# Performance work log

Measured on AMD Instinct MI355X. Metric: run time of the kernel, lower is better.

Reference implementation:

```python
import jax, jax.numpy as jnp
import numpy as np
import math

IN_CH = 1024
OUT_CH = 1024
QK_DIM = 512
NHEADS = 8
NDIM = QK_DIM // NHEADS  # 64 per-head qk dim
VDIM = OUT_CH // NHEADS  # 128 per-head value dim
SCALE = 1.0 / math.sqrt(NDIM)


def setup_inputs() -> dict:
    key = jax.random.key(0)
    ks = jax.random.split(key, 7)
    B, N = 4, 2048
    x = jax.random.normal(ks[0], (B, N, IN_CH), dtype=jnp.float32)
    # Linear weights stored as [in, out] so y = x @ W + b
    s_in = 1.0 / math.sqrt(IN_CH)
    Wq = jax.random.uniform(ks[1], (IN_CH, QK_DIM), jnp.float32, -s_in, s_in)
    bq = jax.random.uniform(ks[2], (QK_DIM,), jnp.float32, -s_in, s_in)
    Wk = jax.random.uniform(ks[3], (IN_CH, QK_DIM), jnp.float32, -s_in, s_in)
    bk = jax.random.uniform(ks[4], (QK_DIM,), jnp.float32, -s_in, s_in)
    Wv = jax.random.uniform(ks[5], (IN_CH, OUT_CH), jnp.float32, -s_in, s_in)
    bv = jax.random.uniform(ks[6], (OUT_CH,), jnp.float32, -s_in, s_in)
    return {"x": x, "Wq": Wq, "bq": bq, "Wk": Wk, "bk": bk, "Wv": Wv, "bv": bv}


def reference(x, Wq, bq, Wk, bk, Wv, bv):
    B, N, C = x.shape
    Q = (x @ Wq + bq).reshape(B, N, NHEADS, NDIM)
    K = (x @ Wk + bk).reshape(B, N, NHEADS, NDIM)
    V = (x @ Wv + bv).reshape(B, N, NHEADS, VDIM)
    # scores: [B, H, N, N]
    scores = jnp.einsum("bnhd,bmhd->bhnm", Q, K) * SCALE
    attn = jax.nn.softmax(scores, axis=-1)
    # message: [B, N, H, VDIM] -> [B, N, OUT_CH]
    msg = jnp.einsum("bhnm,bmhv->bnhv", attn, V)
    return msg.reshape(B, N, OUT_CH)
```

## Files before the change

kernel.cpp:

```cpp
#include <hip/hip_runtime.h>
#include <hip/hip_bf16.h>
#include <math.h>


using bf16 = __hip_bfloat16;
typedef __attribute__((ext_vector_type(4))) short bf16x4;
typedef __attribute__((ext_vector_type(8))) short short8;
typedef __attribute__((ext_vector_type(4))) float f32x4;
typedef __attribute__((ext_vector_type(16))) float f32x16;
typedef __attribute__((ext_vector_type(2))) unsigned int uintx2;

#define C2 0.18033688011112042f

__device__ __forceinline__ void async_ld16(const void* g, void* l) {
  __builtin_amdgcn_global_load_lds(
      (const __attribute__((address_space(1))) unsigned int*)g,
      (__attribute__((address_space(3))) unsigned int*)l, 16, 0, 0);
}

__global__ __launch_bounds__(256) void convert_x(const float* __restrict__ x,
                                                 bf16* __restrict__ xb)
{
  const int i = (blockIdx.x * 256 + threadIdx.x) * 8;
  const float4 a = *(const float4*)(x + i);
  const float4 b = *(const float4*)(x + i + 4);
  union { bf16 h[8]; short8 s; } u;
  u.h[0] = __float2bfloat16(a.x); u.h[1] = __float2bfloat16(a.y);
  u.h[2] = __float2bfloat16(a.z); u.h[3] = __float2bfloat16(a.w);
  u.h[4] = __float2bfloat16(b.x); u.h[5] = __float2bfloat16(b.y);
  u.h[6] = __float2bfloat16(b.z); u.h[7] = __float2bfloat16(b.w);
  *(short8*)(xb + i) = u.s;
}

__global__ __launch_bounds__(256) void transpose_weights(
    const float* __restrict__ Wq, const float* __restrict__ Wk,
    const float* __restrict__ Wv, bf16* __restrict__ Wt)
{
  __shared__ __align__(16) bf16 t[32][33];
  const int i0 = blockIdx.x * 32;
  const int o0 = blockIdx.y * 32;
  const int tx = threadIdx.x & 31, ty = threadIdx.x >> 5;
#pragma unroll
  for (int s = 0; s < 32; s += 8) {
    const int i = i0 + ty + s;
    const int o = o0 + tx;
    const float w = (o < 512)  ? Wq[(size_t)i * 512 + o]
                  : (o < 1024) ? Wk[(size_t)i * 512 + (o - 512)]
                               : Wv[(size_t)i * 1024 + (o - 1024)];
    t[ty + s][tx] = __float2bfloat16(w);
  }
  __syncthreads();
#pragma unroll
  for (int s = 0; s < 32; s += 8)
    Wt[(size_t)(o0 + ty + s) * 1024 + i0 + tx] = t[tx][ty + s];
}

__global__ __launch_bounds__(256, 2) void qkv_gemm(
    const bf16* __restrict__ xb, const bf16* __restrict__ Wt,
    const float* __restrict__ bq, const float* __restrict__ bk,
    const float* __restrict__ bv, bf16* __restrict__ QKV, bf16* __restrict__ Vt)
{
  __shared__ __align__(16) bf16 As[2][8192];
  __shared__ __align__(16) bf16 Bs[2][8192];
  const int tid = threadIdx.x;
  const int w = tid >> 6, lane = tid & 63, quad = lane >> 4, l16 = lane & 15;
  const int m0 = blockIdx.y * 128, n0 = blockIdx.x * 128;
  const int wm = (w >> 1) * 64, wn = (w & 1) * 64;

  const int srow = tid >> 3;
  const int sc   = (tid & 7) ^ (srow & 7);
  const bf16* xg = xb + (size_t)(m0 + srow) * 1024 + sc * 8;
  const bf16* wg = Wt + (size_t)(n0 + srow) * 1024 + sc * 8;
  const int ldb = tid * 16;

  f32x4 acc[4][4];
  const f32x4 z4 = {0.f, 0.f, 0.f, 0.f};
#pragma unroll
  for (int mi = 0; mi < 4; ++mi)
#pragma unroll
    for (int ni = 0; ni < 4; ++ni) acc[mi][ni] = z4;

#define QSTAGE(BUF) do {                                                     \
  async_ld16(xg,         (char*)As[BUF] + ldb);                              \
  async_ld16(xg + 32768, (char*)As[BUF] + ldb + 4096);                       \
  async_ld16(xg + 65536, (char*)As[BUF] + ldb + 8192);                       \
  async_ld16(xg + 98304, (char*)As[BUF] + ldb + 12288);                      \
  async_ld16(wg,         (char*)Bs[BUF] + ldb);                              \
  async_ld16(wg + 32768, (char*)Bs[BUF] + ldb + 4096);                       \
  async_ld16(wg + 65536, (char*)Bs[BUF] + ldb + 8192);                       \
  async_ld16(wg + 98304, (char*)Bs[BUF] + ldb + 12288);                      \
  xg += 64; wg += 64;                                                        \
} while (0)

#define QCOMP(BUF) do {                                                      \
  _Pragma("unroll") for (int kk = 0; kk < 2; ++kk) {                         \
    short8 af[4], bfr[4];                                                    \
    _Pragma("unroll") for (int mi = 0; mi < 4; ++mi) {                       \
      const int row = wm + mi * 16 + l16;                                    \
      const int p = ((kk << 2) | quad) ^ (row & 7);                          \
      af[mi] = *(const short8*)&As[BUF][row * 64 + p * 8];                   \
    }                                                                        \
    _Pragma("unroll") for (int ni = 0; ni < 4; ++ni) {                       \
      const int row = wn + ni * 16 + l16;                                    \
      const int p = ((kk << 2) | quad) ^ (row & 7);                          \
      bfr[ni] = *(const short8*)&Bs[BUF][row * 64 + p * 8];                  \
    }                                                                        \
    _Pragma("unroll") for (int mi = 0; mi < 4; ++mi)                         \
      _Pragma("unroll") for (int ni = 0; ni < 4; ++ni)                       \
        acc[mi][ni] = __builtin_amdgcn_mfma_f32_16x16x32_bf16(af[mi], bfr[ni], acc[mi][ni], 0, 0, 0); \
  }                                                                          \
} while (0)

#define QBODY(BUF, DO_STAGE) do {                                            \
  if (DO_STAGE) {                                                            \
    QSTAGE((BUF) ^ 1);                                                       \
    asm volatile("s_waitcnt vmcnt(8)" ::: "memory");                         \
  } else {                                                                   \
    asm volatile("s_waitcnt vmcnt(0)" ::: "memory");                         \
  }                                                                          \
  __builtin_amdgcn_s_barrier();                                              \
  __builtin_amdgcn_sched_barrier(0);                                         \
  QCOMP(BUF);                                                                \
  asm volatile("s_waitcnt lgkmcnt(0)" ::: "memory");                         \
  __builtin_amdgcn_s_barrier();                                              \
  __builtin_amdgcn_sched_barrier(0);                                         \
} while (0)

  QSTAGE(0);
  for (int u = 0; u < 7; ++u) {
    QBODY(0, true);
    QBODY(1, true);
  }
  QBODY(0, true);
  asm volatile("s_waitcnt vmcnt(0)" ::: "memory");
  __builtin_amdgcn_s_barrier();
  __builtin_amdgcn_sched_barrier(0);
  QCOMP(1);

#undef QSTAGE
#undef QCOMP
#undef QBODY

  if (n0 < 1024) {
#pragma unroll
    for (int ni = 0; ni < 4; ++ni) {
      const int colg = n0 + wn + ni * 16 + l16;
      const float bias = colg < 512 ? bq[colg] : bk[colg - 512];
      const float scl = (colg >= 512) ? C2 : 1.0f;
#pragma unroll
      for (int mi = 0; mi < 4; ++mi)
#pragma unroll
        for (int reg = 0; reg < 4; ++reg) {
          const int rowg = m0 + wm + mi * 16 + quad * 4 + reg;
          QKV[(size_t)rowg * 2048 + colg] = __float2bfloat16((acc[mi][ni][reg] + bias) * scl);
        }
    }
  } else {
#pragma unroll
    for (int ni = 0; ni < 4; ++ni) {
      const int v = n0 - 1024 + wn + ni * 16 + l16;
      const float bias = bv[v];
#pragma unroll
      for (int mi = 0; mi < 4; ++mi) {
        const int rowg0 = m0 + wm + mi * 16 + quad * 4;
        union { bf16 h[4]; bf16x4 s; } u;
#pragma unroll
        for (int reg = 0; reg < 4; ++reg)
          u.h[reg] = __float2bfloat16(acc[mi][ni][reg] + bias);
        *(bf16x4*)(Vt + (size_t)v * 8192 + rowg0) = u.s;
      }
    }
  }
}

__global__ __launch_bounds__(256, 2) void flash_attn(
    const bf16* __restrict__ QKV, const bf16* __restrict__ Vt, float* __restrict__ out)
{
  __shared__ __align__(16) bf16 smem[3 * 12288];
  char* smemc = (char*)smem;
  const int tid = threadIdx.x;
  const int w = tid >> 6, lane = tid & 63, l31 = lane & 31, hi = lane >> 5;
  const int q0 = blockIdx.x * 128;
  const int h  = blockIdx.y;
  const size_t tb = (size_t)blockIdx.z * 2048;

  short8 qf[4];
  const int qrow = w * 32 + l31;
  const bf16* qptr = QKV + (tb + q0 + qrow) * 2048 + h * 64 + hi * 8;
#pragma unroll
  for (int dd = 0; dd < 4; ++dd)
    qf[dd] = *(const short8*)(qptr + dd * 16);

  int adr[4];
#pragma unroll
  for (int i = 0; i < 4; ++i)
    adr[i] = l31 * 128 + (((2 * i + hi) ^ (l31 & 7)) * 16);

  const bf16* kg[2]; int kldo[2];
#pragma unroll
  for (int i = 0; i < 2; ++i) {
    const int L = i * 256 + tid, row = L >> 3, c = (L & 7) ^ (row & 7);
    kg[i] = QKV + (tb + row) * 2048 + 512 + h * 64 + c * 8;
    kldo[i] = L * 16;
  }
  const bf16* vg[4]; int vldo[4];
#pragma unroll
  for (int i = 0; i < 4; ++i) {
    const int L = i * 256 + tid, row = L >> 3, c = (L & 7) ^ (row & 7);
    vg[i] = Vt + (size_t)(h * 128 + row) * 8192 + tb + c * 8;
    vldo[i] = L * 16;
  }

  f32x16 O[4];
#pragma unroll
  for (int t = 0; t < 4; ++t)
#pragma unroll
    for (int e = 0; e < 16; ++e) O[t][e] = 0.f;
  f32x16 Z;
#pragma unroll
  for (int e = 0; e < 16; ++e) Z[e] = 0.f;
  float2 rs; rs.x = 0.f; rs.y = 0.f;

#define STAGE(B) do {                                                        \
  _Pragma("unroll") for (int i = 0; i < 2; ++i) {                            \
    async_ld16(kg[i], smemc + (B) * 24576 + kldo[i]); kg[i] += 131072; }     \
  _Pragma("unroll") for (int i = 0; i < 4; ++i) {                            \
    async_ld16(vg[i], smemc + (B) * 24576 + 8192 + vldo[i]); vg[i] += 64; }  \
} while (0)

#define SOFTPV(B, KT, SV) do {                                               \
  unsigned int pk[8];                                                        \
  _Pragma("unroll") for (int dw = 0; dw < 8; ++dw) {                         \
    const float e0 = exp2f(SV[2 * dw]);                                      \
    const float e1 = exp2f(SV[2 * dw + 1]);                                  \
    rs.x += e0; rs.y += e1;                                                  \
    union { bf16 hh[2]; unsigned int u; } cc;                                \
    cc.hh[0] = __float2bfloat16(e0); cc.hh[1] = __float2bfloat16(e1);        \
    pk[dw] = cc.u; }                                                         \
  _Pragma("unroll") for (int half = 0; half < 2; ++half) {                   \
    const int kc = 2 * (KT) + half; const int b4 = half * 4;                 \
    const uintx2 s0 = __builtin_amdgcn_permlane32_swap(pk[b4], pk[b4 + 2], false, false);     \
    const uintx2 s1 = __builtin_amdgcn_permlane32_swap(pk[b4 + 1], pk[b4 + 3], false, false); \
    union { unsigned int d[4]; short8 v; } pf;                               \
    pf.d[0] = s0.x; pf.d[1] = s1.x; pf.d[2] = s0.y; pf.d[3] = s1.y;          \
    _Pragma("unroll") for (int vt = 0; vt < 4; ++vt) {                       \
      const short8 vf = *(const short8*)(smemc + (B) * 24576 + 8192 + vt * 4096 + adr[kc]); \
      O[vt] = __builtin_amdgcn_mfma_f32_32x32x16_bf16(vf, pf.v, O[vt], 0, 0, 0); } }        \
} while (0)

#define COMPUTE(B) do {                                                      \
  __builtin_amdgcn_s_setprio(1);                                            \
  short8 kf; f32x16 S0, S1;                                                  \
  kf = *(const short8*)(smemc + (B) * 24576 + adr[0]);                       \
  S0 = __builtin_amdgcn_mfma_f32_32x32x16_bf16(kf, qf[0], Z, 0, 0, 0);       \
  kf = *(const short8*)(smemc + (B) * 24576 + adr[1]);                       \
  S0 = __builtin_amdgcn_mfma_f32_32x32x16_bf16(kf, qf[1], S0, 0, 0, 0);      \
  kf = *(const short8*)(smemc + (B) * 24576 + adr[2]);                       \
  S0 = __builtin_amdgcn_mfma_f32_32x32x16_bf16(kf, qf[2], S0, 0, 0, 0);      \
  kf = *(const short8*)(smemc + (B) * 24576 + adr[3]);                       \
  S0 = __builtin_amdgcn_mfma_f32_32x32x16_bf16(kf, qf[3], S0, 0, 0, 0);      \
  kf = *(const short8*)(smemc + (B) * 24576 + 4096 + adr[0]);                \
  S1 = __builtin_amdgcn_mfma_f32_32x32x16_bf16(kf, qf[0], Z, 0, 0, 0);       \
  kf = *(const short8*)(smemc + (B) * 24576 + 4096 + adr[1]);                \
  S1 = __builtin_amdgcn_mfma_f32_32x32x16_bf16(kf, qf[1], S1, 0, 0, 0);      \
  kf = *(const short8*)(smemc + (B) * 24576 + 4096 + adr[2]);                \
  S1 = __builtin_amdgcn_mfma_f32_32x32x16_bf16(kf, qf[2], S1, 0, 0, 0);      \
  kf = *(const short8*)(smemc + (B) * 24576 + 4096 + adr[3]);                \
  S1 = __builtin_amdgcn_mfma_f32_32x32x16_bf16(kf, qf[3], S1, 0, 0, 0);      \
  SOFTPV(B, 0, S0);                                                          \
  SOFTPV(B, 1, S1);                                                          \
  __builtin_amdgcn_s_setprio(0);                                            \
} while (0)

#define PIPE_SYNC6 do {                                                      \
  asm volatile("s_waitcnt vmcnt(6)" ::: "memory");                           \
  __builtin_amdgcn_s_barrier();                                              \
  __builtin_amdgcn_sched_barrier(0);                                         \
} while (0)

  STAGE(0); STAGE(1);
  PIPE_SYNC6;
  for (int u = 0; u < 10; ++u) {
    STAGE(2); COMPUTE(0); PIPE_SYNC6;
    STAGE(0); COMPUTE(1); PIPE_SYNC6;
    STAGE(1); COMPUTE(2); PIPE_SYNC6;
  }
  COMPUTE(0);
  asm volatile("s_waitcnt vmcnt(0)" ::: "memory");
  __builtin_amdgcn_s_barrier();
  __builtin_amdgcn_sched_barrier(0);
  COMPUTE(1);

#undef STAGE
#undef SOFTPV
#undef COMPUTE
#undef PIPE_SYNC6

  float l_run = rs.x + rs.y;
  l_run += __shfl_xor(l_run, 32, 64);

  const float inv_l = 1.0f / l_run;
  float* tbuf = (float*)smem;
  const int qg = tid >> 1;
  const int part = tid & 1;
  for (int vt = 0; vt < 4; ++vt) {
    __syncthreads();
#pragma unroll
    for (int e = 0; e < 16; ++e) {
      const int vl = (e & 3) + 8 * (e >> 2) + 4 * hi;
      tbuf[vl * 132 + w * 32 + l31] = O[vt][e] * inv_l;
    }
    __syncthreads();
    float* dst = out + (tb + q0 + qg) * 1024 + h * 128 + vt * 32 + part * 16;
#pragma unroll
    for (int i = 0; i < 4; ++i) {
      float4 v4;
      v4.x = tbuf[(part * 16 + 4 * i + 0) * 132 + qg];
      v4.y = tbuf[(part * 16 + 4 * i + 1) * 132 + qg];
      v4.z = tbuf[(part * 16 + 4 * i + 2) * 132 + qg];
      v4.w = tbuf[(part * 16 + 4 * i + 3) * 132 + qg];
      *(float4*)(dst + 4 * i) = v4;
    }
  }
}

extern "C" void kernel_launch(void* const* d_in, const int* in_sizes, int n_in,
                              void* d_out, int out_size, void* d_ws, size_t ws_size,
                              hipStream_t stream) {
  const float* x  = (const float*)d_in[0];
  const float* Wq = (const float*)d_in[1];
  const float* bq = (const float*)d_in[2];
  const float* Wk = (const float*)d_in[3];
  const float* bk = (const float*)d_in[4];
  const float* Wv = (const float*)d_in[5];
  const float* bv = (const float*)d_in[6];
  float* out = (float*)d_out;

  char* ws = (char*)d_ws;
  bf16* QKV = (bf16*)ws;
  bf16* Vt  = (bf16*)(ws + 33554432);
  bf16* Wt  = (bf16*)(ws + 33554432 + 16777216);
  bf16* xb  = (bf16*)(ws + 33554432 + 16777216 + 4194304);

  convert_x<<<dim3(4096), 256, 0, stream>>>(x, xb);
  transpose_weights<<<dim3(32, 64), 256, 0, stream>>>(Wq, Wk, Wv, Wt);
  qkv_gemm<<<dim3(16, 64), 256, 0, stream>>>(xb, Wt, bq, bk, bv, QKV, Vt);
  flash_attn<<<dim3(16, 8, 4), 256, 0, stream>>>(QKV, Vt, out);
}
```

Measured before the change: 212.6 us.

## Double query rows per wave in flash attention to reuse K/V fragments

Each wave now processes two 32-row query tiles, so every K and V fragment loaded from shared memory feeds two MFMAs. The query block grows to 256 rows and the grid halves, with launch bounds lowered to one block per CU to allow the extra accumulator registers. This is meant to cut LDS traffic and global K/V loads per unit of work. The cost is higher register pressure and lower occupancy, which reduces latency hiding, and the fewer blocks give a less even fill of the CUs.

```diff
diff --git a/kernel.cpp b/kernel.cpp
--- a/kernel.cpp
+++ b/kernel.cpp
@@ -173,23 +173,25 @@
   }
 }
 
-__global__ __launch_bounds__(256, 2) void flash_attn(
+__global__ __launch_bounds__(256, 1) void flash_attn(
     const bf16* __restrict__ QKV, const bf16* __restrict__ Vt, float* __restrict__ out)
 {
   __shared__ __align__(16) bf16 smem[3 * 12288];
   char* smemc = (char*)smem;
   const int tid = threadIdx.x;
   const int w = tid >> 6, lane = tid & 63, l31 = lane & 31, hi = lane >> 5;
-  const int q0 = blockIdx.x * 128;
+  const int q0 = blockIdx.x * 256;
   const int h  = blockIdx.y;
   const size_t tb = (size_t)blockIdx.z * 2048;
 
-  short8 qf[4];
-  const int qrow = w * 32 + l31;
-  const bf16* qptr = QKV + (tb + q0 + qrow) * 2048 + h * 64 + hi * 8;
-#pragma unroll
-  for (int dd = 0; dd < 4; ++dd)
-    qf[dd] = *(const short8*)(qptr + dd * 16);
+  short8 qfa[4], qfb[4];
+  const bf16* qpa = QKV + (tb + q0 + w * 64 + l31) * 2048 + h * 64 + hi * 8;
+  const bf16* qpb = qpa + 32 * 2048;
+#pragma unroll
+  for (int dd = 0; dd < 4; ++dd) {
+    qfa[dd] = *(const short8*)(qpa + dd * 16);
+    qfb[dd] = *(const short8*)(qpb + dd * 16);
+  }
 
   int adr[4];
 #pragma unroll
@@ -211,15 +213,16 @@
     vldo[i] = L * 16;
   }
 
-  f32x16 O[4];
+  f32x16 Oa[4], Ob[4];
 #pragma unroll
   for (int t = 0; t < 4; ++t)
 #pragma unroll
-    for (int e = 0; e < 16; ++e) O[t][e] = 0.f;
+    for (int e = 0; e < 16; ++e) { Oa[t][e] = 0.f; Ob[t][e] = 0.f; }
   f32x16 Z;
 #pragma unroll
   for (int e = 0; e < 16; ++e) Z[e] = 0.f;
-  float2 rs; rs.x = 0.f; rs.y = 0.f;
+  float2 rsa, rsb;
+  rsa.x = 0.f; rsa.y = 0.f; rsb.x = 0.f; rsb.y = 0.f;
 
 #define STAGE(B) do {                                                        \
   _Pragma("unroll") for (int i = 0; i < 2; ++i) {                            \
@@ -228,48 +231,67 @@
     async_ld16(vg[i], smemc + (B) * 24576 + 8192 + vldo[i]); vg[i] += 64; }  \
 } while (0)
 
-#define SOFTPV(B, KT, SV) do {                                               \
-  unsigned int pk[8];                                                        \
+#define SOFTPV2(B, KT, SA, SB) do {                                          \
+  unsigned int pka[8], pkb[8];                                               \
   _Pragma("unroll") for (int dw = 0; dw < 8; ++dw) {                         \
-    const float e0 = exp2f(SV[2 * dw]);                                      \
-    const float e1 = exp2f(SV[2 * dw + 1]);                                  \
-    rs.x += e0; rs.y += e1;                                                  \
-    union { bf16 hh[2]; unsigned int u; } cc;                                \
-    cc.hh[0] = __float2bfloat16(e0); cc.hh[1] = __float2bfloat16(e1);        \
-    pk[dw] = cc.u; }                                                         \
+    const float a0 = exp2f(SA[2 * dw]);                                      \
+    const float a1 = exp2f(SA[2 * dw + 1]);                                  \
+    rsa.x += a0; rsa.y += a1;                                                \
+    union { bf16 hh[2]; unsigned int u; } ca;                                \
+    ca.hh[0] = __float2bfloat16(a0); ca.hh[1] = __float2bfloat16(a1);        \
+    pka[dw] = ca.u;                                                          \
+    const float b0 = exp2f(SB[2 * dw]);                                      \
+    const float b1 = exp2f(SB[2 * dw + 1]);                                  \
+    rsb.x += b0; rsb.y += b1;                                                \
+    union { bf16 hh[2]; unsigned int u; } cb;                                \
+    cb.hh[0] = __float2bfloat16(b0); cb.hh[1] = __float2bfloat16(b1);        \
+    pkb[dw] = cb.u; }                                                        \
   _Pragma("unroll") for (int half = 0; half < 2; ++half) {                   \
     const int kc = 2 * (KT) + half; const int b4 = half * 4;                 \
-    const uintx2 s0 = __builtin_amdgcn_permlane32_swap(pk[b4], pk[b4 + 2], false, false);     \
-    const uintx2 s1 = __builtin_amdgcn_permlane32_swap(pk[b4 + 1], pk[b4 + 3], false, false); \
-    union { unsigned int d[4]; short8 v; } pf;                               \
-    pf.d[0] = s0.x; pf.d[1] = s1.x; pf.d[2] = s0.y; pf.d[3] = s1.y;          \
+    const uintx2 sa0 = __builtin_amdgcn_permlane32_swap(pka[b4], pka[b4 + 2], false, false);     \
+    const uintx2 sa1 = __builtin_amdgcn_permlane32_swap(pka[b4 + 1], pka[b4 + 3], false, false); \
+    union { unsigned int d[4]; short8 v; } pfa;                              \
+    pfa.d[0] = sa0.x; pfa.d[1] = sa1.x; pfa.d[2] = sa0.y; pfa.d[3] = sa1.y;  \
+    const uintx2 sb0 = __builtin_amdgcn_permlane32_swap(pkb[b4], pkb[b4 + 2], false, false);     \
+    const uintx2 sb1 = __builtin_amdgcn_permlane32_swap(pkb[b4 + 1], pkb[b4 + 3], false, false); \
+    union { unsigned int d[4]; short8 v; } pfb;                              \
+    pfb.d[0] = sb0.x; pfb.d[1] = sb1.x; pfb.d[2] = sb0.y; pfb.d[3] = sb1.y;  \
     _Pragma("unroll") for (int vt = 0; vt < 4; ++vt) {                       \
       const short8 vf = *(const short8*)(smemc + (B) * 24576 + 8192 + vt * 4096 + adr[kc]); \
-      O[vt] = __builtin_amdgcn_mfma_f32_32x32x16_bf16(vf, pf.v, O[vt], 0, 0, 0); } }        \
+      Oa[vt] = __builtin_amdgcn_mfma_f32_32x32x16_bf16(vf, pfa.v, Oa[vt], 0, 0, 0);         \
+      Ob[vt] = __builtin_amdgcn_mfma_f32_32x32x16_bf16(vf, pfb.v, Ob[vt], 0, 0, 0); } }     \
 } while (0)
 
 #define COMPUTE(B) do {                                                      \
-  __builtin_amdgcn_s_setprio(1);                                            \
-  short8 kf; f32x16 S0, S1;                                                  \
+  __builtin_amdgcn_s_setprio(1);                                             \
+  short8 kf; f32x16 S0a, S0b, S1a, S1b;                                      \
   kf = *(const short8*)(smemc + (B) * 24576 + adr[0]);                       \
-  S0 = __builtin_amdgcn_mfma_f32_32x32x16_bf16(kf, qf[0], Z, 0, 0, 0);       \
+  S0a = __builtin_amdgcn_mfma_f32_32x32x16_bf16(kf, qfa[0], Z, 0, 0, 0);     \
+  S0b = __builtin_amdgcn_mfma_f32_32x32x16_bf16(kf, qfb[0], Z, 0, 0, 0);     \
   kf = *(const short8*)(smemc + (B) * 24576 + adr[1]);                       \
-  S0 = __builtin_amdgcn_mfma_f32_32x32x16_bf16(kf, qf[1], S0, 0, 0, 0);      \
+  S0a = __builtin_amdgcn_mfma_f32_32x32x16_bf16(kf, qfa[1], S0a, 0, 0, 0);   \
+  S0b = __builtin_amdgcn_mfma_f32_32x32x16_bf16(kf, qfb[1], S0b, 0, 0, 0);   \
   kf = *(const short8*)(smemc + (B) * 24576 + adr[2]);                       \
-  S0 = __builtin_amdgcn_mfma_f32_32x32x16_bf16(kf, qf[2], S0, 0, 0, 0);      \
+  S0a = __builtin_amdgcn_mfma_f32_32x32x16_bf16(kf, qfa[2], S0a, 0, 0, 0);   \
+  S0b = __builtin_amdgcn_mfma_f32_32x32x16_bf16(kf, qfb[2], S0b, 0, 0, 0);   \
   kf = *(const short8*)(smemc + (B) * 24576 + adr[3]);                       \
-  S0 = __builtin_amdgcn_mfma_f32_32x32x16_bf16(kf, qf[3], S0, 0, 0, 0);      \
+  S0a = __builtin_amdgcn_mfma_f32_32x32x16_bf16(kf, qfa[3], S0a, 0, 0, 0);   \
+  S0b = __builtin_amdgcn_mfma_f32_32x32x16_bf16(kf, qfb[3], S0b, 0, 0, 0);   \
   kf = *(const short8*)(smemc + (B) * 24576 + 4096 + adr[0]);                \
-  S1 = __builtin_amdgcn_mfma_f32_32x32x16_bf16(kf, qf[0], Z, 0, 0, 0);       \
+  S1a = __builtin_amdgcn_mfma_f32_32x32x16_bf16(kf, qfa[0], Z, 0, 0, 0);     \
+  S1b = __builtin_amdgcn_mfma_f32_32x32x16_bf16(kf, qfb[0], Z, 0, 0, 0);     \
   kf = *(const short8*)(smemc + (B) * 24576 + 4096 + adr[1]);                \
-  S1 = __builtin_amdgcn_mfma_f32_32x32x16_bf16(kf, qf[1], S1, 0, 0, 0);      \
+  S1a = __builtin_amdgcn_mfma_f32_32x32x16_bf16(kf, qfa[1], S1a, 0, 0, 0);   \
+  S1b = __builtin_amdgcn_mfma_f32_32x32x16_bf16(kf, qfb[1], S1b, 0, 0, 0);   \
   kf = *(const short8*)(smemc + (B) * 24576 + 4096 + adr[2]);                \
-  S1 = __builtin_amdgcn_mfma_f32_32x32x16_bf16(kf, qf[2], S1, 0, 0, 0);      \
+  S1a = __builtin_amdgcn_mfma_f32_32x32x16_bf16(kf, qfa[2], S1a, 0, 0, 0);   \
+  S1b = __builtin_amdgcn_mfma_f32_32x32x16_bf16(kf, qfb[2], S1b, 0, 0, 0);   \
   kf = *(const short8*)(smemc + (B) * 24576 + 4096 + adr[3]);                \
-  S1 = __builtin_amdgcn_mfma_f32_32x32x16_bf16(kf, qf[3], S1, 0, 0, 0);      \
-  SOFTPV(B, 0, S0);                                                          \
-  SOFTPV(B, 1, S1);                                                          \
-  __builtin_amdgcn_s_setprio(0);                                            \
+  S1a = __builtin_amdgcn_mfma_f32_32x32x16_bf16(kf, qfa[3], S1a, 0, 0, 0);   \
+  S1b = __builtin_amdgcn_mfma_f32_32x32x16_bf16(kf, qfb[3], S1b, 0, 0, 0);   \
+  SOFTPV2(B, 0, S0a, S0b);                                                   \
+  SOFTPV2(B, 1, S1a, S1b);                                                   \
+  __builtin_amdgcn_s_setprio(0);                                             \
 } while (0)
 
 #define PIPE_SYNC6 do {                                                      \
@@ -292,14 +314,17 @@
   COMPUTE(1);
 
 #undef STAGE
-#undef SOFTPV
+#undef SOFTPV2
 #undef COMPUTE
 #undef PIPE_SYNC6
 
-  float l_run = rs.x + rs.y;
-  l_run += __shfl_xor(l_run, 32, 64);
-
-  const float inv_l = 1.0f / l_run;
+  float la = rsa.x + rsa.y;
+  la += __shfl_xor(la, 32, 64);
+  float lb = rsb.x + rsb.y;
+  lb += __shfl_xor(lb, 32, 64);
+  const float inv_a = 1.0f / la;
+  const float inv_b = 1.0f / lb;
+
   float* tbuf = (float*)smem;
   const int qg = tid >> 1;
   const int part = tid & 1;
@@ -308,18 +333,22 @@
 #pragma unroll
     for (int e = 0; e < 16; ++e) {
       const int vl = (e & 3) + 8 * (e >> 2) + 4 * hi;
-      tbuf[vl * 132 + w * 32 + l31] = O[vt][e] * inv_l;
+      tbuf[vl * 260 + w * 64 + l31]      = Oa[vt][e] * inv_a;
+      tbuf[vl * 260 + w * 64 + 32 + l31] = Ob[vt][e] * inv_b;
     }
     __syncthreads();
-    float* dst = out + (tb + q0 + qg) * 1024 + h * 128 + vt * 32 + part * 16;
-#pragma unroll
-    for (int i = 0; i < 4; ++i) {
-      float4 v4;
-      v4.x = tbuf[(part * 16 + 4 * i + 0) * 132 + qg];
-      v4.y = tbuf[(part * 16 + 4 * i + 1) * 132 + qg];
-      v4.z = tbuf[(part * 16 + 4 * i + 2) * 132 + qg];
-      v4.w = tbuf[(part * 16 + 4 * i + 3) * 132 + qg];
-      *(float4*)(dst + 4 * i) = v4;
+#pragma unroll
+    for (int qh = 0; qh < 2; ++qh) {
+      float* dst = out + (tb + q0 + qh * 128 + qg) * 1024 + h * 128 + vt * 32 + part * 16;
+#pragma unroll
+      for (int i = 0; i < 4; ++i) {
+        float4 v4;
+        v4.x = tbuf[(part * 16 + 4 * i + 0) * 260 + qh * 128 + qg];
+        v4.y = tbuf[(part * 16 + 4 * i + 1) * 260 + qh * 128 + qg];
+        v4.z = tbuf[(part * 16 + 4 * i + 2) * 260 + qh * 128 + qg];
+        v4.w = tbuf[(part * 16 + 4 * i + 3) * 260 + qh * 128 + qg];
+        *(float4*)(dst + 4 * i) = v4;
+      }
     }
   }
 }
@@ -345,5 +374,5 @@
   convert_x<<<dim3(4096), 256, 0, stream>>>(x, xb);
   transpose_weights<<<dim3(32, 64), 256, 0, stream>>>(Wq, Wk, Wv, Wt);
   qkv_gemm<<<dim3(16, 64), 256, 0, stream>>>(xb, Wt, bq, bk, bv, QKV, Vt);
-  flash_attn<<<dim3(16, 8, 4), 256, 0, stream>>>(QKV, Vt, out);
-}
+  flash_attn<<<dim3(8, 8, 4), 256, 0, stream>>>(QKV, Vt, out);
+}
```

Measured after the change: 224.4 us. 5.6% more time.

## Use 64x128 tiles and triple-buffered LDS pipeline in QKV GEMM

Applied to the files above, without the earlier changes.

Halves the M tile of the QKV projection GEMM from 128 to 64 rows, doubling the grid to 2048 blocks. It also replaces the double-buffered loop, which had two barriers per K-step, with a three-stage async LDS ring that keeps two tiles in flight and uses one barrier per step. The goal is better latency hiding and more even work spread across CUs. The cost is lower arithmetic intensity per block, more global traffic for the weight operand, and fewer MFMAs per wave between syncs.

```diff
diff --git a/kernel.cpp b/kernel.cpp
--- a/kernel.cpp
+++ b/kernel.cpp
@@ -60,86 +60,87 @@
     const float* __restrict__ bq, const float* __restrict__ bk,
     const float* __restrict__ bv, bf16* __restrict__ QKV, bf16* __restrict__ Vt)
 {
-  __shared__ __align__(16) bf16 As[2][8192];
-  __shared__ __align__(16) bf16 Bs[2][8192];
+  __shared__ __align__(16) bf16 smem[3 * 12288];
+  char* smemc = (char*)smem;
   const int tid = threadIdx.x;
   const int w = tid >> 6, lane = tid & 63, quad = lane >> 4, l16 = lane & 15;
-  const int m0 = blockIdx.y * 128, n0 = blockIdx.x * 128;
-  const int wm = (w >> 1) * 64, wn = (w & 1) * 64;
-
-  const int srow = tid >> 3;
-  const int sc   = (tid & 7) ^ (srow & 7);
-  const bf16* xg = xb + (size_t)(m0 + srow) * 1024 + sc * 8;
-  const bf16* wg = Wt + (size_t)(n0 + srow) * 1024 + sc * 8;
-  const int ldb = tid * 16;
-
-  f32x4 acc[4][4];
+  const int m0 = blockIdx.y * 64, n0 = blockIdx.x * 128;
+  const int wm = (w >> 1) * 32, wn = (w & 1) * 64;
+
+  const bf16* ag[2]; int aldo[2];
+#pragma unroll
+  for (int i = 0; i < 2; ++i) {
+    const int L = i * 256 + tid, row = L >> 3, c = (L & 7) ^ (row & 7);
+    ag[i] = xb + (size_t)(m0 + row) * 1024 + c * 8;
+    aldo[i] = L * 16;
+  }
+  const bf16* bg[4]; int bldo[4];
+#pragma unroll
+  for (int i = 0; i < 4; ++i) {
+    const int L = i * 256 + tid, row = L >> 3, c = (L & 7) ^ (row & 7);
+    bg[i] = Wt + (size_t)(n0 + row) * 1024 + c * 8;
+    bldo[i] = L * 16;
+  }
+
+  f32x4 acc[2][4];
   const f32x4 z4 = {0.f, 0.f, 0.f, 0.f};
 #pragma unroll
-  for (int mi = 0; mi < 4; ++mi)
+  for (int mi = 0; mi < 2; ++mi)
 #pragma unroll
     for (int ni = 0; ni < 4; ++ni) acc[mi][ni] = z4;
 
-#define QSTAGE(BUF) do {                                                     \
-  async_ld16(xg,         (char*)As[BUF] + ldb);                              \
-  async_ld16(xg + 32768, (char*)As[BUF] + ldb + 4096);                       \
-  async_ld16(xg + 65536, (char*)As[BUF] + ldb + 8192);                       \
-  async_ld16(xg + 98304, (char*)As[BUF] + ldb + 12288);                      \
-  async_ld16(wg,         (char*)Bs[BUF] + ldb);                              \
-  async_ld16(wg + 32768, (char*)Bs[BUF] + ldb + 4096);                       \
-  async_ld16(wg + 65536, (char*)Bs[BUF] + ldb + 8192);                       \
-  async_ld16(wg + 98304, (char*)Bs[BUF] + ldb + 12288);                      \
-  xg += 64; wg += 64;                                                        \
-} while (0)
-
-#define QCOMP(BUF) do {                                                      \
+#define QSTAGE(B) do {                                                       \
+  _Pragma("unroll") for (int i = 0; i < 2; ++i) {                            \
+    async_ld16(ag[i], smemc + (B) * 24576 + aldo[i]); ag[i] += 64; }         \
+  _Pragma("unroll") for (int i = 0; i < 4; ++i) {                            \
+    async_ld16(bg[i], smemc + (B) * 24576 + 8192 + bldo[i]); bg[i] += 64; }  \
+} while (0)
+
+#define QCOMP(B) do {                                                        \
+  const char* Ab = smemc + (B) * 24576;                                      \
+  const char* Bb = smemc + (B) * 24576 + 8192;                               \
   _Pragma("unroll") for (int kk = 0; kk < 2; ++kk) {                         \
-    short8 af[4], bfr[4];                                                    \
-    _Pragma("unroll") for (int mi = 0; mi < 4; ++mi) {                       \
+    short8 af[2], bfr[4];                                                    \
+    _Pragma("unroll") for (int mi = 0; mi < 2; ++mi) {                       \
       const int row = wm + mi * 16 + l16;                                    \
       const int p = ((kk << 2) | quad) ^ (row & 7);                          \
-      af[mi] = *(const short8*)&As[BUF][row * 64 + p * 8];                   \
+      af[mi] = *(const short8*)(Ab + row * 128 + p * 16);                    \
     }                                                                        \
     _Pragma("unroll") for (int ni = 0; ni < 4; ++ni) {                       \
       const int row = wn + ni * 16 + l16;                                    \
       const int p = ((kk << 2) | quad) ^ (row & 7);                          \
-      bfr[ni] = *(const short8*)&Bs[BUF][row * 64 + p * 8];                  \
+      bfr[ni] = *(const short8*)(Bb + row * 128 + p * 16);                   \
     }                                                                        \
-    _Pragma("unroll") for (int mi = 0; mi < 4; ++mi)                         \
+    _Pragma("unroll") for (int mi = 0; mi < 2; ++mi)                         \
       _Pragma("unroll") for (int ni = 0; ni < 4; ++ni)                       \
         acc[mi][ni] = __builtin_amdgcn_mfma_f32_16x16x32_bf16(af[mi], bfr[ni], acc[mi][ni], 0, 0, 0); \
   }                                                                          \
 } while (0)
 
-#define QBODY(BUF, DO_STAGE) do {                                            \
-  if (DO_STAGE) {                                                            \
-    QSTAGE((BUF) ^ 1);                                                       \
-    asm volatile("s_waitcnt vmcnt(8)" ::: "memory");                         \
-  } else {                                                                   \
-    asm volatile("s_waitcnt vmcnt(0)" ::: "memory");                         \
-  }                                                                          \
+#define QSYNC6 do {                                                          \
+  asm volatile("s_waitcnt vmcnt(6)" ::: "memory");                           \
   __builtin_amdgcn_s_barrier();                                              \
   __builtin_amdgcn_sched_barrier(0);                                         \
-  QCOMP(BUF);                                                                \
-  asm volatile("s_waitcnt lgkmcnt(0)" ::: "memory");                         \
-  __builtin_amdgcn_s_barrier();                                              \
-  __builtin_amdgcn_sched_barrier(0);                                         \
-} while (0)
-
-  QSTAGE(0);
-  for (int u = 0; u < 7; ++u) {
-    QBODY(0, true);
-    QBODY(1, true);
-  }
-  QBODY(0, true);
+} while (0)
+
+  QSTAGE(0); QSTAGE(1);
+  QSYNC6;
+  for (int u = 0; u < 4; ++u) {
+    QSTAGE(2); QCOMP(0); QSYNC6;
+    QSTAGE(0); QCOMP(1); QSYNC6;
+    QSTAGE(1); QCOMP(2); QSYNC6;
+  }
+  QSTAGE(2); QCOMP(0); QSYNC6;
+  QSTAGE(0); QCOMP(1); QSYNC6;
+  QCOMP(2);
   asm volatile("s_waitcnt vmcnt(0)" ::: "memory");
   __builtin_amdgcn_s_barrier();
   __builtin_amdgcn_sched_barrier(0);
-  QCOMP(1);
+  QCOMP(0);
 
 #undef QSTAGE
 #undef QCOMP
-#undef QBODY
+#undef QSYNC6
 
   if (n0 < 1024) {
 #pragma unroll
@@ -148,7 +149,7 @@
       const float bias = colg < 512 ? bq[colg] : bk[colg - 512];
       const float scl = (colg >= 512) ? C2 : 1.0f;
 #pragma unroll
-      for (int mi = 0; mi < 4; ++mi)
+      for (int mi = 0; mi < 2; ++mi)
 #pragma unroll
         for (int reg = 0; reg < 4; ++reg) {
           const int rowg = m0 + wm + mi * 16 + quad * 4 + reg;
@@ -161,7 +162,7 @@
       const int v = n0 - 1024 + wn + ni * 16 + l16;
       const float bias = bv[v];
 #pragma unroll
-      for (int mi = 0; mi < 4; ++mi) {
+      for (int mi = 0; mi < 2; ++mi) {
         const int rowg0 = m0 + wm + mi * 16 + quad * 4;
         union { bf16 h[4]; bf16x4 s; } u;
 #pragma unroll
@@ -344,6 +345,6 @@
 
   convert_x<<<dim3(4096), 256, 0, stream>>>(x, xb);
   transpose_weights<<<dim3(32, 64), 256, 0, stream>>>(Wq, Wk, Wv, Wt);
-  qkv_gemm<<<dim3(16, 64), 256, 0, stream>>>(xb, Wt, bq, bk, bv, QKV, Vt);
+  qkv_gemm<<<dim3(16, 128), 256, 0, stream>>>(xb, Wt, bq, bk, bv, QKV, Vt);
   flash_attn<<<dim3(16, 8, 4), 256, 0, stream>>>(QKV, Vt, out);
 }
```

After: 211.8 us. No clear change (-0.4%).
